# Performance work log

Hardware: AMD Instinct MI355X
Metric: run time of the kernel (lower is better)

The kernel has to match this reference:

```python
import jax, jax.numpy as jnp
import numpy as np

GAMMA = 1.0  # matches init_kwargs gamma
B, N, M = 128, 512, 512


def setup_inputs() -> dict:
    key = jax.random.key(0)
    D = jax.random.uniform(key, (B, N, M), dtype=jnp.float32)
    return {"D": D}


def _softmin3(a, b, c, gamma):
    # soft_min over the 3 DP neighbors: -gamma * logsumexp(-x/gamma)
    z = jnp.stack([a, b, c], axis=0) * (-1.0 / gamma)
    return -gamma * jax.nn.logsumexp(z, axis=0)


def reference(D):
    """Soft-DTW forward: returns R[:, N, M], shape (B,).
    DP over rows (lax.scan), inner scan over columns carries R[i, j-1].
    Vectorized over the batch dimension.
    """
    gamma = GAMMA
    b, n, m = D.shape
    dt = D.dtype
    inf = jnp.array(jnp.inf, dt)

    def row_step(prev_row, d_row):
        # prev_row: (b, m+1) = R[i-1, 0..m]; d_row: (b, m) = D[:, i-1, :]
        def col_step(left, xs):
            diag, up, d = xs  # each (b,)
            new = d + _softmin3(diag, up, left, gamma)
            return new, new
        xs = (prev_row[:, :-1].T, prev_row[:, 1:].T, d_row.T)  # each (m, b)
        _, outs = jax.lax.scan(col_step, jnp.full((b,), inf, dt), xs)
        new_row = jnp.concatenate([jnp.full((b, 1), inf, dt), outs.T], axis=1)
        return new_row, None

    # R[0, :] = [0, inf, inf, ...]
    init = jnp.concatenate([jnp.zeros((b, 1), dt), jnp.full((b, m), inf, dt)], axis=1)
    final_row, _ = jax.lax.scan(row_step, init, jnp.swapaxes(D, 0, 1))  # scan over rows (n, b, m)
    return final_row[:, -1]
```

## Files before the change

### kernel.cpp

```cpp
#include <hip/hip_runtime.h>


#define BB 128
#define NN 512
#define MM 512
#define L2E 1.4426950408889634f
#define LN2 0.6931471805599453f

__device__ __forceinline__ int iclamp(int x, int lo, int hi) {
    return x < lo ? lo : (x > hi ? hi : x);
}

template<int CTRL>
__device__ __forceinline__ float dpp_fmax(float v) {
    const int s = __builtin_amdgcn_update_dpp(
        __float_as_int(v), __float_as_int(v), CTRL, 0xF, 0xF, false);
    return __builtin_fmaxf(v, __int_as_float(s));
}

template<int P, int U>
__device__ __forceinline__ void dostep(
    const float* __restrict__ Db, const int lane, const int w,
    const int jb, const int sbase, const int tq,
    float (&r1)[2], float (&r2)[2], float2 (&buf)[2][8],
    int& irow, float& sh, float& shprev, float& bl, float& bd,
    float* ring, const float scale)
{
    {
        const int r = iclamp(irow, 0, NN - 1);
        buf[P ^ 1][U] = *(const float2*)(Db + ((r << 9) + jb));
        irow += 1;
    }
    const int s = sbase + P * 8 + U;

    float nv1;
    {
        constexpr int par  = (U >= 1) ? P : (P ^ 1);
        constexpr int slot = (U >= 1) ? (U - 1) : 7;
        const float d = buf[par][slot].y;
        float wgt = __builtin_amdgcn_exp2f(-L2E * d);
        const bool junk = (s - 1) >= tq;
        wgt = junk ? 0.0f : wgt;
        nv1 = wgt * ((r1[1] + r1[0]) + r2[0]);
    }
    if (lane == 63 && w < 3) ring[(w << 6) + (s & 63)] = nv1;

    float nv0;
    {
        const float lf = (lane == 0) ? bl : sh;
        const float dg = (lane == 0) ? bd : shprev;
        const float d  = buf[P][U].x;
        float wgt = __builtin_amdgcn_exp2f(-L2E * d);
        const bool junk = s >= tq;
        wgt = junk ? 0.0f : wgt;
        nv0 = wgt * ((r1[0] + lf) + dg);
    }

    r2[0] = r1[0]; r2[1] = r1[1];
    r1[0] = nv0;   r1[1] = nv1;
    bd = bl;
    shprev = sh;
    sh = __shfl_up(r1[1], 1, 64);
    if (w > 0) bl = ring[((w - 1) << 6) + (s & 63)] * scale;
}

__device__ __forceinline__ void renorm_local(
    float (&r1)[2], float (&r2)[2], float& sh, float& shprev,
    float& bl, float& bd, float& gexp)
{
    float m = __builtin_fmaxf(r1[0], r1[1]);
    m = dpp_fmax<0x111>(m);
    m = dpp_fmax<0x112>(m);
    m = dpp_fmax<0x114>(m);
    m = dpp_fmax<0x118>(m);
    m = dpp_fmax<0x142>(m);
    m = dpp_fmax<0x143>(m);
    const int mb = __builtin_amdgcn_readlane(__float_as_int(m), 63);
    const int eb = (mb >> 23) & 255;
    const int ex = (eb > 0 && eb < 255) ? (eb - 127) : 0;
    const float rs = __int_as_float((127 - ex) << 23);
    r1[0] *= rs; r1[1] *= rs; r2[0] *= rs; r2[1] *= rs;
    sh *= rs; shprev *= rs;
    bl *= rs;
    bd *= rs;
    gexp += (float)ex;
}

#define S8(PP) \
    dostep<PP,0>(Db,lane,w,jb,sbase,tq,r1,r2,buf,irow,sh,shprev,bl,bd,ring,scale); \
    dostep<PP,1>(Db,lane,w,jb,sbase,tq,r1,r2,buf,irow,sh,shprev,bl,bd,ring,scale); \
    dostep<PP,2>(Db,lane,w,jb,sbase,tq,r1,r2,buf,irow,sh,shprev,bl,bd,ring,scale); \
    dostep<PP,3>(Db,lane,w,jb,sbase,tq,r1,r2,buf,irow,sh,shprev,bl,bd,ring,scale); \
    dostep<PP,4>(Db,lane,w,jb,sbase,tq,r1,r2,buf,irow,sh,shprev,bl,bd,ring,scale); \
    dostep<PP,5>(Db,lane,w,jb,sbase,tq,r1,r2,buf,irow,sh,shprev,bl,bd,ring,scale); \
    dostep<PP,6>(Db,lane,w,jb,sbase,tq,r1,r2,buf,irow,sh,shprev,bl,bd,ring,scale); \
    dostep<PP,7>(Db,lane,w,jb,sbase,tq,r1,r2,buf,irow,sh,shprev,bl,bd,ring,scale);

__launch_bounds__(256, 1)
__global__ void softdtw_skew4(const float* __restrict__ D, float* __restrict__ out) {
    const int b = blockIdx.x;
    const int tid = (int)threadIdx.x;
    const int w = tid >> 6;
    const int lane = tid & 63;
    const int jb = (w << 7) + (lane << 1);
    const int tq = jb + NN;
    const float* __restrict__ Db = D + (size_t)b * (NN * MM);

    __shared__ float ringS[3 * 64];
    __shared__ float gxS[8];
    float* ring = ringS;
    float* gx = gxS;

    if (tid < 3 * 64) ringS[tid] = 0.0f;
    if (tid < 8) gxS[tid] = 0.0f;

    float r1[2] = {0.0f, 0.0f};
    float r2[2] = {0.0f, 0.0f};
    float2 buf[2][8];
    #pragma unroll
    for (int v = 0; v < 8; ++v) buf[1][v] = make_float2(0.0f, 0.0f);
    #pragma unroll
    for (int v = 0; v < 8; ++v) {
        const int r = iclamp(v - jb, 0, NN - 1);
        buf[0][v] = *(const float2*)(Db + ((r << 9) + jb));
    }
    int irow = 8 - jb;
    float sh = 0.0f, shprev = 0.0f;
    float bl = 0.0f;
    float bd = (w == 0) ? 1.0f : 0.0f;
    float gexp = 0.0f;

    #pragma unroll 1
    for (int k = 0; k < 67; ++k) {
        asm volatile("s_waitcnt lgkmcnt(0)" ::: "memory");
        __builtin_amdgcn_s_barrier();
        asm volatile("" ::: "memory");
        const int kw = k - w;
        if (kw < 0 || kw > 63) continue;
        const int sbase = kw << 4;
        renorm_local(r1, r2, sh, shprev, bl, bd, gexp);
        if (lane == 63 && w < 3) gx[(w << 1) + (k & 1)] = gexp;
        float scale = 1.0f;
        if (w > 0) {
            const float gxp = gx[((w - 1) << 1) + ((k - 1) & 1)];
            int dlt = (int)(gxp - gexp);
            dlt = iclamp(dlt, -126, 126);
            scale = __int_as_float((127 + dlt) << 23);
        }
        if (kw < 63) {
            S8(0)
            S8(1)
        } else {
            S8(0)
            dostep<1,0>(Db,lane,w,jb,sbase,tq,r1,r2,buf,irow,sh,shprev,bl,bd,ring,scale);
            dostep<1,1>(Db,lane,w,jb,sbase,tq,r1,r2,buf,irow,sh,shprev,bl,bd,ring,scale);
            dostep<1,2>(Db,lane,w,jb,sbase,tq,r1,r2,buf,irow,sh,shprev,bl,bd,ring,scale);
            dostep<1,3>(Db,lane,w,jb,sbase,tq,r1,r2,buf,irow,sh,shprev,bl,bd,ring,scale);
            dostep<1,4>(Db,lane,w,jb,sbase,tq,r1,r2,buf,irow,sh,shprev,bl,bd,ring,scale);
            dostep<1,5>(Db,lane,w,jb,sbase,tq,r1,r2,buf,irow,sh,shprev,bl,bd,ring,scale);
            dostep<1,6>(Db,lane,w,jb,sbase,tq,r1,r2,buf,irow,sh,shprev,bl,bd,ring,scale);
        }
    }

    if (w == 3 && lane == 63) {
        out[b] = -(__builtin_amdgcn_logf(r1[1]) + gexp) * LN2;
    }
}

extern "C" void kernel_launch(void* const* d_in, const int* in_sizes, int n_in,
                              void* d_out, int out_size, void* d_ws, size_t ws_size,
                              hipStream_t stream) {
    const float* D = (const float*)d_in[0];
    float* out = (float*)d_out;
    softdtw_skew4<<<BB, 256, 0, stream>>>(D, out);
}
```

Before: 377.2 us.

## Batch inter-wave boundary exchange into vector LDS transfers per chunk

The kernel used to send each wave's last-lane boundary value to the next wave through one LDS store per DP step, with a matching scalar LDS load per step. Now each wave keeps its 16 boundary values per chunk in registers and writes them, plus its exponent, with four ds_write_b128 instructions at the end of the chunk. The consumer reads them with four ds_read_b128 once at the chunk start and pre-scales them into a register array. The cross-lane neighbour shift also moves from __shfl_up to a DPP wave_shr:1. Together these take LDS latency and bpermute traffic off the serial per-step dependency chain, at the cost of extra registers, inline asm, and uninitialised LDS reads that are masked for wave 0.

New measurement: 328.6 us. 12.9% less time.

```diff
diff --git a/kernel.cpp b/kernel.cpp
--- a/kernel.cpp
+++ b/kernel.cpp
@@ -7,6 +7,8 @@
 #define L2E 1.4426950408889634f
 #define LN2 0.6931471805599453f
 
+typedef float f32x4 __attribute__((ext_vector_type(4)));
+
 __device__ __forceinline__ int iclamp(int x, int lo, int hi) {
     return x < lo ? lo : (x > hi ? hi : x);
 }
@@ -18,13 +20,19 @@
     return __builtin_fmaxf(v, __int_as_float(s));
 }
 
+__device__ __forceinline__ float dpp_shr1(float v) {
+    const int s = __builtin_amdgcn_update_dpp(
+        __float_as_int(v), __float_as_int(v), 0x138, 0xF, 0xF, false);
+    return __int_as_float(s);
+}
+
 template<int P, int U>
 __device__ __forceinline__ void dostep(
-    const float* __restrict__ Db, const int lane, const int w,
-    const int jb, const int sbase, const int tq,
+    const float* __restrict__ Db, const int lane, const int jb,
+    const int sbase, const int tq,
     float (&r1)[2], float (&r2)[2], float2 (&buf)[2][8],
     int& irow, float& sh, float& shprev, float& bl, float& bd,
-    float* ring, const float scale)
+    const float (&blv)[16], float (&hist)[16])
 {
     {
         const int r = iclamp(irow, 0, NN - 1);
@@ -39,11 +47,10 @@
         constexpr int slot = (U >= 1) ? (U - 1) : 7;
         const float d = buf[par][slot].y;
         float wgt = __builtin_amdgcn_exp2f(-L2E * d);
-        const bool junk = (s - 1) >= tq;
-        wgt = junk ? 0.0f : wgt;
+        wgt = ((s - 1) >= tq) ? 0.0f : wgt;
         nv1 = wgt * ((r1[1] + r1[0]) + r2[0]);
     }
-    if (lane == 63 && w < 3) ring[(w << 6) + (s & 63)] = nv1;
+    hist[P * 8 + U] = nv1;
 
     float nv0;
     {
@@ -51,17 +58,16 @@
         const float dg = (lane == 0) ? bd : shprev;
         const float d  = buf[P][U].x;
         float wgt = __builtin_amdgcn_exp2f(-L2E * d);
-        const bool junk = s >= tq;
-        wgt = junk ? 0.0f : wgt;
+        wgt = (s >= tq) ? 0.0f : wgt;
         nv0 = wgt * ((r1[0] + lf) + dg);
     }
 
     r2[0] = r1[0]; r2[1] = r1[1];
     r1[0] = nv0;   r1[1] = nv1;
     bd = bl;
+    bl = blv[P * 8 + U];
     shprev = sh;
-    sh = __shfl_up(r1[1], 1, 64);
-    if (w > 0) bl = ring[((w - 1) << 6) + (s & 63)] * scale;
+    sh = dpp_shr1(r1[1]);
 }
 
 __device__ __forceinline__ void renorm_local(
@@ -87,17 +93,17 @@
 }
 
 #define S8(PP) \
-    dostep<PP,0>(Db,lane,w,jb,sbase,tq,r1,r2,buf,irow,sh,shprev,bl,bd,ring,scale); \
-    dostep<PP,1>(Db,lane,w,jb,sbase,tq,r1,r2,buf,irow,sh,shprev,bl,bd,ring,scale); \
-    dostep<PP,2>(Db,lane,w,jb,sbase,tq,r1,r2,buf,irow,sh,shprev,bl,bd,ring,scale); \
-    dostep<PP,3>(Db,lane,w,jb,sbase,tq,r1,r2,buf,irow,sh,shprev,bl,bd,ring,scale); \
-    dostep<PP,4>(Db,lane,w,jb,sbase,tq,r1,r2,buf,irow,sh,shprev,bl,bd,ring,scale); \
-    dostep<PP,5>(Db,lane,w,jb,sbase,tq,r1,r2,buf,irow,sh,shprev,bl,bd,ring,scale); \
-    dostep<PP,6>(Db,lane,w,jb,sbase,tq,r1,r2,buf,irow,sh,shprev,bl,bd,ring,scale); \
-    dostep<PP,7>(Db,lane,w,jb,sbase,tq,r1,r2,buf,irow,sh,shprev,bl,bd,ring,scale);
+    dostep<PP,0>(Db,lane,jb,sbase,tq,r1,r2,buf,irow,sh,shprev,bl,bd,blv,hist); \
+    dostep<PP,1>(Db,lane,jb,sbase,tq,r1,r2,buf,irow,sh,shprev,bl,bd,blv,hist); \
+    dostep<PP,2>(Db,lane,jb,sbase,tq,r1,r2,buf,irow,sh,shprev,bl,bd,blv,hist); \
+    dostep<PP,3>(Db,lane,jb,sbase,tq,r1,r2,buf,irow,sh,shprev,bl,bd,blv,hist); \
+    dostep<PP,4>(Db,lane,jb,sbase,tq,r1,r2,buf,irow,sh,shprev,bl,bd,blv,hist); \
+    dostep<PP,5>(Db,lane,jb,sbase,tq,r1,r2,buf,irow,sh,shprev,bl,bd,blv,hist); \
+    dostep<PP,6>(Db,lane,jb,sbase,tq,r1,r2,buf,irow,sh,shprev,bl,bd,blv,hist); \
+    dostep<PP,7>(Db,lane,jb,sbase,tq,r1,r2,buf,irow,sh,shprev,bl,bd,blv,hist);
 
 __launch_bounds__(256, 1)
-__global__ void softdtw_skew4(const float* __restrict__ D, float* __restrict__ out) {
+__global__ void softdtw_skew4c(const float* __restrict__ D, float* __restrict__ out) {
     const int b = blockIdx.x;
     const int tid = (int)threadIdx.x;
     const int w = tid >> 6;
@@ -106,13 +112,13 @@
     const int tq = jb + NN;
     const float* __restrict__ Db = D + (size_t)b * (NN * MM);
 
-    __shared__ float ringS[3 * 64];
-    __shared__ float gxS[8];
-    float* ring = ringS;
-    float* gx = gxS;
-
-    if (tid < 3 * 64) ringS[tid] = 0.0f;
-    if (tid < 8) gxS[tid] = 0.0f;
+    __shared__ __align__(16) float ldsF[264];
+    const unsigned ldsbase = (unsigned)(size_t)(void*)ldsF;
+    const int rw = (w > 0) ? (w - 1) : 0;
+    const unsigned rchunk = ldsbase + ((unsigned)rw << 8);
+    const unsigned rgx    = ldsbase + 1024u + ((unsigned)rw << 3);
+    const unsigned wchunk = ldsbase + ((unsigned)w << 8);
+    const unsigned wgx    = ldsbase + 1024u + ((unsigned)w << 3);
 
     float r1[2] = {0.0f, 0.0f};
     float r2[2] = {0.0f, 0.0f};
@@ -132,33 +138,85 @@
 
     #pragma unroll 1
     for (int k = 0; k < 67; ++k) {
-        asm volatile("s_waitcnt lgkmcnt(0)" ::: "memory");
-        __builtin_amdgcn_s_barrier();
-        asm volatile("" ::: "memory");
+        asm volatile("s_waitcnt lgkmcnt(0)\n\ts_barrier");
         const int kw = k - w;
         if (kw < 0 || kw > 63) continue;
         const int sbase = kw << 4;
+
+        f32x4 q0, q1, q2, q3; float gxp;
+        {
+            const unsigned raddr = rchunk + (((unsigned)sbase & 63u) << 2);
+            const unsigned gaddr = rgx + (((unsigned)(k - 1) & 1u) << 2);
+            asm volatile(
+                "ds_read_b128 %0, %5\n\t"
+                "ds_read_b128 %1, %5 offset:16\n\t"
+                "ds_read_b128 %2, %5 offset:32\n\t"
+                "ds_read_b128 %3, %5 offset:48\n\t"
+                "ds_read_b32  %4, %6\n\t"
+                "s_waitcnt lgkmcnt(0)"
+                : "=&v"(q0), "=&v"(q1), "=&v"(q2), "=&v"(q3), "=&v"(gxp)
+                : "v"(raddr), "v"(gaddr));
+        }
+
         renorm_local(r1, r2, sh, shprev, bl, bd, gexp);
-        if (lane == 63 && w < 3) gx[(w << 1) + (k & 1)] = gexp;
-        float scale = 1.0f;
-        if (w > 0) {
-            const float gxp = gx[((w - 1) << 1) + ((k - 1) & 1)];
+
+        float scale;
+        {
             int dlt = (int)(gxp - gexp);
             dlt = iclamp(dlt, -126, 126);
             scale = __int_as_float((127 + dlt) << 23);
         }
+        const bool act = (w > 0);
+        float blv[16];
+        blv[ 0] = act ? q0.x * scale : 0.0f;
+        blv[ 1] = act ? q0.y * scale : 0.0f;
+        blv[ 2] = act ? q0.z * scale : 0.0f;
+        blv[ 3] = act ? q0.w * scale : 0.0f;
+        blv[ 4] = act ? q1.x * scale : 0.0f;
+        blv[ 5] = act ? q1.y * scale : 0.0f;
+        blv[ 6] = act ? q1.z * scale : 0.0f;
+        blv[ 7] = act ? q1.w * scale : 0.0f;
+        blv[ 8] = act ? q2.x * scale : 0.0f;
+        blv[ 9] = act ? q2.y * scale : 0.0f;
+        blv[10] = act ? q2.z * scale : 0.0f;
+        blv[11] = act ? q2.w * scale : 0.0f;
+        blv[12] = act ? q3.x * scale : 0.0f;
+        blv[13] = act ? q3.y * scale : 0.0f;
+        blv[14] = act ? q3.z * scale : 0.0f;
+        blv[15] = act ? q3.w * scale : 0.0f;
+
+        float hist[16];
+        hist[15] = 0.0f;
+
         if (kw < 63) {
             S8(0)
             S8(1)
         } else {
             S8(0)
-            dostep<1,0>(Db,lane,w,jb,sbase,tq,r1,r2,buf,irow,sh,shprev,bl,bd,ring,scale);
-            dostep<1,1>(Db,lane,w,jb,sbase,tq,r1,r2,buf,irow,sh,shprev,bl,bd,ring,scale);
-            dostep<1,2>(Db,lane,w,jb,sbase,tq,r1,r2,buf,irow,sh,shprev,bl,bd,ring,scale);
-            dostep<1,3>(Db,lane,w,jb,sbase,tq,r1,r2,buf,irow,sh,shprev,bl,bd,ring,scale);
-            dostep<1,4>(Db,lane,w,jb,sbase,tq,r1,r2,buf,irow,sh,shprev,bl,bd,ring,scale);
-            dostep<1,5>(Db,lane,w,jb,sbase,tq,r1,r2,buf,irow,sh,shprev,bl,bd,ring,scale);
-            dostep<1,6>(Db,lane,w,jb,sbase,tq,r1,r2,buf,irow,sh,shprev,bl,bd,ring,scale);
+            dostep<1,0>(Db,lane,jb,sbase,tq,r1,r2,buf,irow,sh,shprev,bl,bd,blv,hist);
+            dostep<1,1>(Db,lane,jb,sbase,tq,r1,r2,buf,irow,sh,shprev,bl,bd,blv,hist);
+            dostep<1,2>(Db,lane,jb,sbase,tq,r1,r2,buf,irow,sh,shprev,bl,bd,blv,hist);
+            dostep<1,3>(Db,lane,jb,sbase,tq,r1,r2,buf,irow,sh,shprev,bl,bd,blv,hist);
+            dostep<1,4>(Db,lane,jb,sbase,tq,r1,r2,buf,irow,sh,shprev,bl,bd,blv,hist);
+            dostep<1,5>(Db,lane,jb,sbase,tq,r1,r2,buf,irow,sh,shprev,bl,bd,blv,hist);
+            dostep<1,6>(Db,lane,jb,sbase,tq,r1,r2,buf,irow,sh,shprev,bl,bd,blv,hist);
+        }
+
+        if (lane == 63 && w < 3) {
+            const unsigned waddr = wchunk + (((unsigned)sbase & 63u) << 2);
+            const unsigned gaddr = wgx + (((unsigned)k & 1u) << 2);
+            const f32x4 h0 = {hist[ 0], hist[ 1], hist[ 2], hist[ 3]};
+            const f32x4 h1 = {hist[ 4], hist[ 5], hist[ 6], hist[ 7]};
+            const f32x4 h2 = {hist[ 8], hist[ 9], hist[10], hist[11]};
+            const f32x4 h3 = {hist[12], hist[13], hist[14], hist[15]};
+            asm volatile(
+                "ds_write_b128 %0, %2\n\t"
+                "ds_write_b128 %0, %3 offset:16\n\t"
+                "ds_write_b128 %0, %4 offset:32\n\t"
+                "ds_write_b128 %0, %5 offset:48\n\t"
+                "ds_write_b32  %1, %6"
+                :: "v"(waddr), "v"(gaddr),
+                   "v"(h0), "v"(h1), "v"(h2), "v"(h3), "v"(gexp));
         }
     }
 
@@ -172,5 +230,5 @@
                               hipStream_t stream) {
     const float* D = (const float*)d_in[0];
     float* out = (float*)d_out;
-    softdtw_skew4<<<BB, 256, 0, stream>>>(D, out);
-}
+    softdtw_skew4c<<<BB, 256, 0, stream>>>(D, out);
+}
```

## Use two waves with four columns per lane and batched LDS boundary exchange

Applied to the files above, without the earlier changes.

Each block now runs two wavefronts instead of four, with every lane owning four columns loaded as float4. This removes two skew stages, so the wavefront pipeline has fewer k iterations. The inter-wave boundary values are read once per 16-step chunk with ds_read_b128 instead of one LDS read per step, and the lane shift uses DPP instead of a shuffle. The cost is a longer serial dependency chain per lane (four columns per step), more registers, and fewer threads per block across the 128 blocks.

Result: faster. 320.2 us (-15.1%).

```diff
diff --git a/kernel.cpp b/kernel.cpp
--- a/kernel.cpp
+++ b/kernel.cpp
@@ -7,6 +7,8 @@
 #define L2E 1.4426950408889634f
 #define LN2 0.6931471805599453f
 
+typedef float f32x4 __attribute__((ext_vector_type(4)));
+
 __device__ __forceinline__ int iclamp(int x, int lo, int hi) {
     return x < lo ? lo : (x > hi ? hi : x);
 }
@@ -18,57 +20,76 @@
     return __builtin_fmaxf(v, __int_as_float(s));
 }
 
-template<int P, int U>
+__device__ __forceinline__ float dpp_shr1(float v) {
+    const int s = __builtin_amdgcn_update_dpp(
+        __float_as_int(v), __float_as_int(v), 0x138, 0xF, 0xF, false);
+    return __int_as_float(s);
+}
+
+template<int T>
 __device__ __forceinline__ void dostep(
-    const float* __restrict__ Db, const int lane, const int w,
+    const float* __restrict__ Db, const int lane, const bool wpub,
     const int jb, const int sbase, const int tq,
-    float (&r1)[2], float (&r2)[2], float2 (&buf)[2][8],
+    float (&r1)[4], float (&r2)[4], float4 (&buf)[16],
     int& irow, float& sh, float& shprev, float& bl, float& bd,
-    float* ring, const float scale)
+    const f32x4 (&bv)[4], const unsigned wrA)
 {
     {
         const int r = iclamp(irow, 0, NN - 1);
-        buf[P ^ 1][U] = *(const float2*)(Db + ((r << 9) + jb));
+        buf[(T + 8) & 15] = *(const float4*)(Db + ((r << 9) + jb));
         irow += 1;
     }
-    const int s = sbase + P * 8 + U;
-
-    float nv1;
-    {
-        constexpr int par  = (U >= 1) ? P : (P ^ 1);
-        constexpr int slot = (U >= 1) ? (U - 1) : 7;
-        const float d = buf[par][slot].y;
-        float wgt = __builtin_amdgcn_exp2f(-L2E * d);
-        const bool junk = (s - 1) >= tq;
-        wgt = junk ? 0.0f : wgt;
-        nv1 = wgt * ((r1[1] + r1[0]) + r2[0]);
-    }
-    if (lane == 63 && w < 3) ring[(w << 6) + (s & 63)] = nv1;
-
-    float nv0;
-    {
+    const int s = sbase + T;
+
+    float nv0, nv1, nv2, nv3;
+    {
+        constexpr int i3 = (16 + T - 3) & 15;
+        const float d = buf[i3].w;
+        float wg = __builtin_amdgcn_exp2f(-L2E * d);
+        wg = ((s - 3) >= tq) ? 0.0f : wg;
+        nv3 = wg * ((r1[3] + r1[2]) + r2[2]);
+    }
+    {
+        constexpr int i2 = (16 + T - 2) & 15;
+        const float d = buf[i2].z;
+        float wg = __builtin_amdgcn_exp2f(-L2E * d);
+        wg = ((s - 2) >= tq) ? 0.0f : wg;
+        nv2 = wg * ((r1[2] + r1[1]) + r2[1]);
+    }
+    {
+        constexpr int i1 = (16 + T - 1) & 15;
+        const float d = buf[i1].y;
+        float wg = __builtin_amdgcn_exp2f(-L2E * d);
+        wg = ((s - 1) >= tq) ? 0.0f : wg;
+        nv1 = wg * ((r1[1] + r1[0]) + r2[0]);
+    }
+    if (wpub)
+        asm volatile("ds_write_b32 %0, %1 offset:%2"
+                     :: "v"(wrA), "v"(nv3), "n"(T * 4));
+    {
+        constexpr int i0 = T & 15;
+        const float d = buf[i0].x;
         const float lf = (lane == 0) ? bl : sh;
         const float dg = (lane == 0) ? bd : shprev;
-        const float d  = buf[P][U].x;
-        float wgt = __builtin_amdgcn_exp2f(-L2E * d);
-        const bool junk = s >= tq;
-        wgt = junk ? 0.0f : wgt;
-        nv0 = wgt * ((r1[0] + lf) + dg);
-    }
-
-    r2[0] = r1[0]; r2[1] = r1[1];
-    r1[0] = nv0;   r1[1] = nv1;
+        float wg = __builtin_amdgcn_exp2f(-L2E * d);
+        wg = (s >= tq) ? 0.0f : wg;
+        nv0 = wg * ((r1[0] + lf) + dg);
+    }
+
+    r2[0] = r1[0]; r2[1] = r1[1]; r2[2] = r1[2]; r2[3] = r1[3];
+    r1[0] = nv0;   r1[1] = nv1;   r1[2] = nv2;   r1[3] = nv3;
     bd = bl;
+    bl = bv[T >> 2][T & 3];
     shprev = sh;
-    sh = __shfl_up(r1[1], 1, 64);
-    if (w > 0) bl = ring[((w - 1) << 6) + (s & 63)] * scale;
+    sh = dpp_shr1(nv3);
 }
 
 __device__ __forceinline__ void renorm_local(
-    float (&r1)[2], float (&r2)[2], float& sh, float& shprev,
+    float (&r1)[4], float (&r2)[4], float& sh, float& shprev,
     float& bl, float& bd, float& gexp)
 {
-    float m = __builtin_fmaxf(r1[0], r1[1]);
+    float m = __builtin_fmaxf(__builtin_fmaxf(r1[0], r1[1]),
+                              __builtin_fmaxf(r1[2], r1[3]));
     m = dpp_fmax<0x111>(m);
     m = dpp_fmax<0x112>(m);
     m = dpp_fmax<0x114>(m);
@@ -79,50 +100,42 @@
     const int eb = (mb >> 23) & 255;
     const int ex = (eb > 0 && eb < 255) ? (eb - 127) : 0;
     const float rs = __int_as_float((127 - ex) << 23);
-    r1[0] *= rs; r1[1] *= rs; r2[0] *= rs; r2[1] *= rs;
+    r1[0] *= rs; r1[1] *= rs; r1[2] *= rs; r1[3] *= rs;
+    r2[0] *= rs; r2[1] *= rs; r2[2] *= rs; r2[3] *= rs;
     sh *= rs; shprev *= rs;
     bl *= rs;
     bd *= rs;
     gexp += (float)ex;
 }
 
-#define S8(PP) \
-    dostep<PP,0>(Db,lane,w,jb,sbase,tq,r1,r2,buf,irow,sh,shprev,bl,bd,ring,scale); \
-    dostep<PP,1>(Db,lane,w,jb,sbase,tq,r1,r2,buf,irow,sh,shprev,bl,bd,ring,scale); \
-    dostep<PP,2>(Db,lane,w,jb,sbase,tq,r1,r2,buf,irow,sh,shprev,bl,bd,ring,scale); \
-    dostep<PP,3>(Db,lane,w,jb,sbase,tq,r1,r2,buf,irow,sh,shprev,bl,bd,ring,scale); \
-    dostep<PP,4>(Db,lane,w,jb,sbase,tq,r1,r2,buf,irow,sh,shprev,bl,bd,ring,scale); \
-    dostep<PP,5>(Db,lane,w,jb,sbase,tq,r1,r2,buf,irow,sh,shprev,bl,bd,ring,scale); \
-    dostep<PP,6>(Db,lane,w,jb,sbase,tq,r1,r2,buf,irow,sh,shprev,bl,bd,ring,scale); \
-    dostep<PP,7>(Db,lane,w,jb,sbase,tq,r1,r2,buf,irow,sh,shprev,bl,bd,ring,scale);
-
-__launch_bounds__(256, 1)
-__global__ void softdtw_skew4(const float* __restrict__ D, float* __restrict__ out) {
+#define DSTEP(T) dostep<T>(Db,lane,wpub,jb,sbase,tq,r1,r2,buf,irow,sh,shprev,bl,bd,bv,wrA);
+
+__launch_bounds__(128, 1)
+__global__ void softdtw_skew2(const float* __restrict__ D, float* __restrict__ out) {
     const int b = blockIdx.x;
     const int tid = (int)threadIdx.x;
     const int w = tid >> 6;
     const int lane = tid & 63;
-    const int jb = (w << 7) + (lane << 1);
+    const int jb = (w << 8) + (lane << 2);
     const int tq = jb + NN;
+    const bool wpub = (w == 0) && (lane == 63);
     const float* __restrict__ Db = D + (size_t)b * (NN * MM);
 
-    __shared__ float ringS[3 * 64];
-    __shared__ float gxS[8];
-    float* ring = ringS;
-    float* gx = gxS;
-
-    if (tid < 3 * 64) ringS[tid] = 0.0f;
-    if (tid < 8) gxS[tid] = 0.0f;
-
-    float r1[2] = {0.0f, 0.0f};
-    float r2[2] = {0.0f, 0.0f};
-    float2 buf[2][8];
-    #pragma unroll
-    for (int v = 0; v < 8; ++v) buf[1][v] = make_float2(0.0f, 0.0f);
+    __shared__ __align__(16) float ldsF[66];
+    const unsigned ldsbase = (unsigned)(size_t)(void*)ldsF;
+    const unsigned ringb = ldsbase;
+    const unsigned gxb   = ldsbase + 256u;
+
+    float r1[4] = {0.0f, 0.0f, 0.0f, 0.0f};
+    float r2[4] = {0.0f, 0.0f, 0.0f, 0.0f};
+    float4 buf[16];
+    buf[13] = make_float4(0.f, 0.f, 0.f, 0.f);
+    buf[14] = make_float4(0.f, 0.f, 0.f, 0.f);
+    buf[15] = make_float4(0.f, 0.f, 0.f, 0.f);
     #pragma unroll
     for (int v = 0; v < 8; ++v) {
         const int r = iclamp(v - jb, 0, NN - 1);
-        buf[0][v] = *(const float2*)(Db + ((r << 9) + jb));
+        buf[v] = *(const float4*)(Db + ((r << 9) + jb));
     }
     int irow = 8 - jb;
     float sh = 0.0f, shprev = 0.0f;
@@ -131,39 +144,65 @@
     float gexp = 0.0f;
 
     #pragma unroll 1
-    for (int k = 0; k < 67; ++k) {
-        asm volatile("s_waitcnt lgkmcnt(0)" ::: "memory");
-        __builtin_amdgcn_s_barrier();
-        asm volatile("" ::: "memory");
+    for (int k = 0; k < 65; ++k) {
+        asm volatile("s_waitcnt lgkmcnt(0)\n\ts_barrier");
         const int kw = k - w;
         if (kw < 0 || kw > 63) continue;
         const int sbase = kw << 4;
+
+        f32x4 q0, q1, q2, q3; float gxp;
+        {
+            const unsigned raddr = ringb + (((unsigned)sbase & 63u) << 2);
+            const unsigned gaddr = gxb + (((unsigned)(k - 1) & 1u) << 2);
+            asm volatile(
+                "ds_read_b128 %0, %5\n\t"
+                "ds_read_b128 %1, %5 offset:16\n\t"
+                "ds_read_b128 %2, %5 offset:32\n\t"
+                "ds_read_b128 %3, %5 offset:48\n\t"
+                "ds_read_b32  %4, %6\n\t"
+                "s_waitcnt lgkmcnt(0)"
+                : "=&v"(q0), "=&v"(q1), "=&v"(q2), "=&v"(q3), "=&v"(gxp)
+                : "v"(raddr), "v"(gaddr));
+        }
+
         renorm_local(r1, r2, sh, shprev, bl, bd, gexp);
-        if (lane == 63 && w < 3) gx[(w << 1) + (k & 1)] = gexp;
-        float scale = 1.0f;
-        if (w > 0) {
-            const float gxp = gx[((w - 1) << 1) + ((k - 1) & 1)];
+
+        if (wpub) {
+            const unsigned ga = gxb + (((unsigned)k & 1u) << 2);
+            asm volatile("ds_write_b32 %0, %1" :: "v"(ga), "v"(gexp));
+        }
+
+        float scale;
+        {
             int dlt = (int)(gxp - gexp);
             dlt = iclamp(dlt, -126, 126);
             scale = __int_as_float((127 + dlt) << 23);
         }
+        const bool act = (w > 0);
+        const f32x4 zz = {0.0f, 0.0f, 0.0f, 0.0f};
+        f32x4 bv[4];
+        bv[0] = act ? q0 * scale : zz;
+        bv[1] = act ? q1 * scale : zz;
+        bv[2] = act ? q2 * scale : zz;
+        bv[3] = act ? q3 * scale : zz;
+
+        const unsigned wrA = ringb + (((unsigned)sbase & 63u) << 2);
+
         if (kw < 63) {
-            S8(0)
-            S8(1)
+            DSTEP(0)  DSTEP(1)  DSTEP(2)  DSTEP(3)
+            DSTEP(4)  DSTEP(5)  DSTEP(6)  DSTEP(7)
+            DSTEP(8)  DSTEP(9)  DSTEP(10) DSTEP(11)
+            DSTEP(12) DSTEP(13) DSTEP(14) DSTEP(15)
         } else {
-            S8(0)
-            dostep<1,0>(Db,lane,w,jb,sbase,tq,r1,r2,buf,irow,sh,shprev,bl,bd,ring,scale);
-            dostep<1,1>(Db,lane,w,jb,sbase,tq,r1,r2,buf,irow,sh,shprev,bl,bd,ring,scale);
-            dostep<1,2>(Db,lane,w,jb,sbase,tq,r1,r2,buf,irow,sh,shprev,bl,bd,ring,scale);
-            dostep<1,3>(Db,lane,w,jb,sbase,tq,r1,r2,buf,irow,sh,shprev,bl,bd,ring,scale);
-            dostep<1,4>(Db,lane,w,jb,sbase,tq,r1,r2,buf,irow,sh,shprev,bl,bd,ring,scale);
-            dostep<1,5>(Db,lane,w,jb,sbase,tq,r1,r2,buf,irow,sh,shprev,bl,bd,ring,scale);
-            dostep<1,6>(Db,lane,w,jb,sbase,tq,r1,r2,buf,irow,sh,shprev,bl,bd,ring,scale);
-        }
-    }
-
-    if (w == 3 && lane == 63) {
-        out[b] = -(__builtin_amdgcn_logf(r1[1]) + gexp) * LN2;
+            DSTEP(0)  DSTEP(1)  DSTEP(2)  DSTEP(3)
+            DSTEP(4)  DSTEP(5)  DSTEP(6)  DSTEP(7)
+            DSTEP(8)  DSTEP(9)  DSTEP(10) DSTEP(11)
+            DSTEP(12) DSTEP(13) DSTEP(14)
+        }
+    }
+
+    if (w == 1 && lane == 63) {
+        out[b] = -(__builtin_amdgcn_logf(r1[3]) + gexp) * LN2;
     }
 }
 
@@ -172,5 +211,5 @@
                               hipStream_t stream) {
     const float* D = (const float*)d_in[0];
     float* out = (float*)d_out;
-    softdtw_skew4<<<BB, 256, 0, stream>>>(D, out);
-}
+    softdtw_skew2<<<BB, 128, 0, stream>>>(D, out);
+}
```
